# Optimization experiments

Hardware: AMD Instinct MI355X
Metric: run time of the kernel (lower is better)

The kernel has to match this reference:

```python
import jax, jax.numpy as jnp
import numpy as np

L, B, D = 512, 4, 1024          # seq(atoms), batch, embed dim
H, DH = 16, 64                  # heads, head dim
FF = 4096                       # ffn hidden
HP = 32                         # encoder_pair_embed_dim
K = 256                         # pbc-expanded atoms


def _ln(x, g, b):
    m = x.mean(-1, keepdims=True)
    v = x.var(-1, keepdims=True)
    return (x - m) / jnp.sqrt(v + 1e-5) * g + b


def _rope(x, pos):
    # x: [S,B,H,DH], pos: [B,S]
    inv_freq = 1.0 / (10000.0 ** (jnp.arange(0, DH, 2, dtype=jnp.float32) / DH))
    ang = pos.astype(jnp.float32)[..., None] * inv_freq          # [B,S,DH/2]
    cos = jnp.cos(ang).transpose(1, 0, 2)[:, :, None, :]          # [S,B,1,DH/2]
    sin = jnp.sin(ang).transpose(1, 0, 2)[:, :, None, :]
    x1, x2 = jnp.split(x, 2, axis=-1)
    return jnp.concatenate([x1 * cos - x2 * sin, x1 * sin + x2 * cos], axis=-1)


def setup_inputs() -> dict:
    key = jax.random.key(0)
    ks = jax.random.split(key, 12)
    s = 0.02
    return dict(
        x=jax.random.normal(ks[0], (L, B, D), jnp.float32),
        x_pair=jax.random.normal(ks[1], (L, L + K, B, HP), jnp.float32),
        padding_mask=jnp.zeros((B, L), bool),
        expand_mask=jnp.zeros((B, K), bool),
        position_ids=jnp.tile(jnp.arange(L, dtype=jnp.int32)[None, :], (B, 1)),
        outcell_index=jax.random.randint(ks[2], (B, K), 0, L, dtype=jnp.int32),
        wq=jax.random.normal(ks[3], (D, D), jnp.float32) * s,
        wk=jax.random.normal(ks[4], (D, D), jnp.float32) * s,
        wv=jax.random.normal(ks[5], (D, D), jnp.float32) * s,
        wo=jax.random.normal(ks[6], (D, D), jnp.float32) * s,
        fc1=jax.random.normal(ks[7], (D, FF), jnp.float32) * s,
        fc2=jax.random.normal(ks[8], (FF, D), jnp.float32) * s,
        top_ln_g=jnp.ones((D,), jnp.float32), top_ln_b=jnp.zeros((D,), jnp.float32),
        mid_ln_g=jnp.ones((D,), jnp.float32), mid_ln_b=jnp.zeros((D,), jnp.float32),
        pair_ln_g=jnp.ones((D,), jnp.float32), pair_ln_b=jnp.zeros((D,), jnp.float32),
        pair_w1=jax.random.normal(ks[9], (D, 2 * HP), jnp.float32) * s,
        pair_w2=jax.random.normal(ks[10], (2 * HP, HP), jnp.float32) * s,
    )


def reference(x, x_pair, padding_mask, expand_mask, position_ids, outcell_index,
              wq, wk, wv, wo, fc1, fc2,
              top_ln_g, top_ln_b, mid_ln_g, mid_ln_b,
              pair_ln_g, pair_ln_b, pair_w1, pair_w2):
    barange = jnp.arange(B)
    # ---- self-attention block (pre-LN, RoPE, pbc-expanded keys/values) ----
    residual = x
    h = _ln(x, top_ln_g, top_ln_b)                               # [L,B,D]
    h_exp = h[outcell_index.T, barange[None, :], :]               # [K,B,D] gather along L per batch
    kv_src = jnp.concatenate([h, h_exp], axis=0)                  # [L+K,B,D]
    q = (h @ wq).reshape(L, B, H, DH)
    k = (kv_src @ wk).reshape(L + K, B, H, DH)
    v = (kv_src @ wv).reshape(L + K, B, H, DH)
    pos_exp = position_ids[barange[:, None], outcell_index]       # [B,K]
    pos_k = jnp.concatenate([position_ids, pos_exp], axis=1)      # [B,L+K]
    q = _rope(q, position_ids)
    k = _rope(k, pos_k)
    scores = jnp.einsum('lbhd,kbhd->bhlk', q, k) / np.sqrt(DH)    # [B,H,L,L+K]
    kp_mask = jnp.concatenate([padding_mask, expand_mask], axis=1)  # [B,L+K]
    scores = jnp.where(kp_mask[:, None, None, :], -1e9, scores)
    attn = jax.nn.softmax(scores, axis=-1)
    o = jnp.einsum('bhlk,kbhd->lbhd', attn, v).reshape(L, B, D) @ wo
    x = residual + o
    # ---- FFN block ----
    residual = x
    h = _ln(x, mid_ln_g, mid_ln_b)
    x = residual + jax.nn.gelu(h @ fc1, approximate=False) @ fc2
    # ---- pair outer product ----
    x_p_i = jax.nn.silu(_ln(x, pair_ln_g, pair_ln_b) @ pair_w1) @ pair_w2   # [L,B,HP]
    expand_x_p_i = x_p_i[outcell_index.T, barange[None, :], :]              # [K,B,HP]
    x_p_j = jnp.concatenate([x_p_i, expand_x_p_i], axis=0)                  # [L+K,B,HP]
    x_pair = x_pair + jnp.einsum('lbh,kbh->lkbh', x_p_i, x_p_j)             # [L,L+K,B,HP]
    return x, x_pair
```

## Files before the change

### kernel.cpp

```cpp
#include <hip/hip_runtime.h>
#include <math.h>


typedef __bf16 bf16x8 __attribute__((ext_vector_type(8)));
typedef float f32x4 __attribute__((ext_vector_type(4)));

__device__ __forceinline__ unsigned short f2bf(float f) {
  unsigned u = __float_as_uint(f);
  u = (u + 0x7fffu + ((u >> 16) & 1u)) >> 16;
  return (unsigned short)u;
}
__device__ __forceinline__ float bf2f(unsigned short s) {
  return __uint_as_float(((unsigned)s) << 16);
}

__device__ __forceinline__ void gload_lds16(const void* g, void* l) {
  __builtin_amdgcn_global_load_lds(
      (__attribute__((address_space(1))) void*)g,
      (__attribute__((address_space(3))) void*)l, 16, 0, 0);
}

__global__ __launch_bounds__(256) void transpose_all(
    const float* __restrict__ wq, const float* __restrict__ wk, const float* __restrict__ wv,
    const float* __restrict__ wo, const float* __restrict__ fc1, const float* __restrict__ fc2,
    unsigned short* __restrict__ qkvT, unsigned short* __restrict__ woT,
    unsigned short* __restrict__ fc1T, unsigned short* __restrict__ fc2T) {
  int id = blockIdx.x;
  const float* W; unsigned short* WT; int Kd, Nd, n0, k0;
  if (id < 3072) {
    int which = id >> 10, lid = id & 1023;
    W = which == 0 ? wq : (which == 1 ? wk : wv);
    WT = qkvT + (long)which * 1024 * 1024;
    Kd = 1024; Nd = 1024; n0 = (lid & 31) * 32; k0 = (lid >> 5) * 32;
  } else if (id < 4096) {
    int lid = id - 3072;
    W = wo; WT = woT; Kd = 1024; Nd = 1024;
    n0 = (lid & 31) * 32; k0 = (lid >> 5) * 32;
  } else if (id < 8192) {
    int lid = id - 4096;
    W = fc1; WT = fc1T; Kd = 1024; Nd = 4096;
    n0 = (lid & 127) * 32; k0 = (lid >> 7) * 32;
  } else {
    int lid = id - 8192;
    W = fc2; WT = fc2T; Kd = 4096; Nd = 1024;
    n0 = (lid & 31) * 32; k0 = (lid >> 5) * 32;
  }
  __shared__ float tile[32][33];
  const int tx = threadIdx.x, ty = threadIdx.y;
#pragma unroll
  for (int i = 0; i < 32; i += 8)
    tile[ty + i][tx] = W[(long)(k0 + ty + i) * Nd + n0 + tx];
  __syncthreads();
#pragma unroll
  for (int i = 0; i < 32; i += 8)
    WT[(long)(n0 + ty + i) * Kd + k0 + tx] = f2bf(tile[tx][ty + i]);
}

__global__ __launch_bounds__(256) void ln_bf16(
    const float* __restrict__ X, unsigned short* __restrict__ Y,
    const float* __restrict__ g, const float* __restrict__ bb) {
  const int row = blockIdx.x, t = threadIdx.x;
  const float* xr = X + (long)row * 1024;
  float v[4]; float s = 0.f, ss = 0.f;
#pragma unroll
  for (int i = 0; i < 4; i++) { v[i] = xr[t + 256 * i]; s += v[i]; ss += v[i] * v[i]; }
#pragma unroll
  for (int o = 32; o > 0; o >>= 1) { s += __shfl_down(s, o); ss += __shfl_down(ss, o); }
  __shared__ float red[8];
  const int wave = t >> 6, lane = t & 63;
  if (lane == 0) { red[wave] = s; red[4 + wave] = ss; }
  __syncthreads();
  s = red[0] + red[1] + red[2] + red[3];
  ss = red[4] + red[5] + red[6] + red[7];
  const float mean = s * (1.f / 1024.f);
  const float rstd = rsqrtf(ss * (1.f / 1024.f) - mean * mean + 1e-5f);
#pragma unroll
  for (int i = 0; i < 4; i++) {
    const int c = t + 256 * i;
    Y[(long)row * 1024 + c] = f2bf((v[i] - mean) * rstd * g[c] + bb[c]);
  }
}

__global__ __launch_bounds__(256) void red_ln(
    const float* __restrict__ p0, const float* __restrict__ p1,
    const float* __restrict__ R, float* __restrict__ Xout,
    const float* __restrict__ g, const float* __restrict__ bb,
    unsigned short* __restrict__ Y) {
  const int row = blockIdx.x, t = threadIdx.x;
  const long base = (long)row * 1024;
  float v[4]; float s = 0.f, ss = 0.f;
#pragma unroll
  for (int i = 0; i < 4; i++) {
    const int c = t + 256 * i;
    float val = p0[base + c] + p1[base + c] + R[base + c];
    Xout[base + c] = val;
    v[i] = val; s += val; ss += val * val;
  }
#pragma unroll
  for (int o = 32; o > 0; o >>= 1) { s += __shfl_down(s, o); ss += __shfl_down(ss, o); }
  __shared__ float red[8];
  const int wave = t >> 6, lane = t & 63;
  if (lane == 0) { red[wave] = s; red[4 + wave] = ss; }
  __syncthreads();
  s = red[0] + red[1] + red[2] + red[3];
  ss = red[4] + red[5] + red[6] + red[7];
  const float mean = s * (1.f / 1024.f);
  const float rstd = rsqrtf(ss * (1.f / 1024.f) - mean * mean + 1e-5f);
#pragma unroll
  for (int i = 0; i < 4; i++) {
    const int c = t + 256 * i;
    Y[base + c] = f2bf((v[i] - mean) * rstd * g[c] + bb[c]);
  }
}

__global__ __launch_bounds__(256) void gather_kv(unsigned short* kv, const int* __restrict__ oc) {
  int idx = blockIdx.x * 256 + threadIdx.x;
  int col4 = idx & 255;
  int r = idx >> 8;
  int j = r >> 2, b = r & 3;
  int src = oc[b * 256 + j] * 4 + b;
  ((ushort4*)kv)[((512 + j) * 4 + b) * 256 + col4] = ((const ushort4*)kv)[src * 256 + col4];
}

template <int EPI>
__global__ __launch_bounds__(256) void gemm_nt(
    const unsigned short* __restrict__ A, const unsigned short* __restrict__ BT,
    void* __restrict__ Cout, const float* __restrict__ R, int M, int N, int Kd) {
  __shared__ __align__(16) unsigned short As[128 * 32];
  __shared__ __align__(16) unsigned short Bs[128 * 32];
  const int t = threadIdx.x;
  const int wave = t >> 6, lane = t & 63;
  const int m0 = blockIdx.y * 128, n0 = blockIdx.x * 128;
  const int wr = wave >> 1, wc = wave & 1;
  const int lr = lane & 15, lg = lane >> 4;

  f32x4 acc[4][4] = {};

  const int srow = 32 * wave + (lane >> 2);
  const int schunk = (lane & 3) * 8;
  const unsigned short* Ag = A + (long)(m0 + srow) * Kd + schunk;
  const unsigned short* Bg = BT + (long)(n0 + srow) * Kd + schunk;
  unsigned short* AsW = &As[(32 * wave) * 32];
  unsigned short* BsW = &Bs[(32 * wave) * 32];

  for (int k0 = 0; k0 < Kd; k0 += 32) {
    __syncthreads();
    gload_lds16(Ag + k0, AsW);
    gload_lds16(Ag + k0 + 16 * (long)Kd, AsW + 16 * 32);
    gload_lds16(Bg + k0, BsW);
    gload_lds16(Bg + k0 + 16 * (long)Kd, BsW + 16 * 32);
    asm volatile("s_waitcnt vmcnt(0)" ::: "memory");
    __syncthreads();

    bf16x8 af[4], bfr[4];
#pragma unroll
    for (int mf = 0; mf < 4; mf++)
      af[mf] = *(const bf16x8*)&As[(64 * wr + 16 * mf + lr) * 32 + lg * 8];
#pragma unroll
    for (int nf = 0; nf < 4; nf++)
      bfr[nf] = *(const bf16x8*)&Bs[(64 * wc + 16 * nf + lr) * 32 + lg * 8];
#pragma unroll
    for (int mf = 0; mf < 4; mf++)
#pragma unroll
      for (int nf = 0; nf < 4; nf++)
        acc[mf][nf] = __builtin_amdgcn_mfma_f32_16x16x32_bf16(af[mf], bfr[nf], acc[mf][nf], 0, 0, 0);
  }

#pragma unroll
  for (int mf = 0; mf < 4; mf++)
#pragma unroll
    for (int nf = 0; nf < 4; nf++)
#pragma unroll
      for (int r = 0; r < 4; r++) {
        const int row = m0 + 64 * wr + 16 * mf + 4 * lg + r;
        const int col = n0 + 64 * wc + 16 * nf + lr;
        const long off = (long)row * N + col;
        float v = acc[mf][nf][r];
        if constexpr (EPI == 1) {
          ((float*)Cout)[off] = v + R[off];
        } else if constexpr (EPI == 2) {
          float gl = 0.5f * v * (1.0f + erff(v * 0.70710678118654752f));
          ((unsigned short*)Cout)[off] = f2bf(gl);
        } else if constexpr (EPI == 3) {
          ((unsigned short*)Cout)[off] = f2bf(v);
        } else {
          ((float*)Cout)[off] = v;
        }
      }
}

__global__ __launch_bounds__(256) void gemm_nt_splitk(
    const unsigned short* __restrict__ A, const unsigned short* __restrict__ BT,
    float* __restrict__ Cp, int M, int N, int Kd) {
  const int kh = Kd >> 1;
  const long kbase = (long)blockIdx.z * kh;
  const unsigned short* A2 = A + kbase;
  const unsigned short* B2 = BT + kbase;
  float* Cz = Cp + (long)blockIdx.z * M * N;

  __shared__ __align__(16) unsigned short As[128 * 32];
  __shared__ __align__(16) unsigned short Bs[128 * 32];
  const int t = threadIdx.x;
  const int wave = t >> 6, lane = t & 63;
  const int m0 = blockIdx.y * 128, n0 = blockIdx.x * 128;
  const int wr = wave >> 1, wc = wave & 1;
  const int lr = lane & 15, lg = lane >> 4;

  f32x4 acc[4][4] = {};

  const int srow = 32 * wave + (lane >> 2);
  const int schunk = (lane & 3) * 8;
  const unsigned short* Ag = A2 + (long)(m0 + srow) * Kd + schunk;
  const unsigned short* Bg = B2 + (long)(n0 + srow) * Kd + schunk;
  unsigned short* AsW = &As[(32 * wave) * 32];
  unsigned short* BsW = &Bs[(32 * wave) * 32];

  for (int k0 = 0; k0 < kh; k0 += 32) {
    __syncthreads();
    gload_lds16(Ag + k0, AsW);
    gload_lds16(Ag + k0 + 16 * (long)Kd, AsW + 16 * 32);
    gload_lds16(Bg + k0, BsW);
    gload_lds16(Bg + k0 + 16 * (long)Kd, BsW + 16 * 32);
    asm volatile("s_waitcnt vmcnt(0)" ::: "memory");
    __syncthreads();

    bf16x8 af[4], bfr[4];
#pragma unroll
    for (int mf = 0; mf < 4; mf++)
      af[mf] = *(const bf16x8*)&As[(64 * wr + 16 * mf + lr) * 32 + lg * 8];
#pragma unroll
    for (int nf = 0; nf < 4; nf++)
      bfr[nf] = *(const bf16x8*)&Bs[(64 * wc + 16 * nf + lr) * 32 + lg * 8];
#pragma unroll
    for (int mf = 0; mf < 4; mf++)
#pragma unroll
      for (int nf = 0; nf < 4; nf++)
        acc[mf][nf] = __builtin_amdgcn_mfma_f32_16x16x32_bf16(af[mf], bfr[nf], acc[mf][nf], 0, 0, 0);
  }

#pragma unroll
  for (int mf = 0; mf < 4; mf++)
#pragma unroll
    for (int nf = 0; nf < 4; nf++)
#pragma unroll
      for (int r = 0; r < 4; r++) {
        const int row = m0 + 64 * wr + 16 * mf + 4 * lg + r;
        const int col = n0 + 64 * wc + 16 * nf + lr;
        Cz[(long)row * N + col] = acc[mf][nf][r];
      }
}

__global__ __launch_bounds__(256) void rope_split2(
    const unsigned short* __restrict__ QKV, const int* __restrict__ pos_ids,
    const int* __restrict__ oc,
    unsigned short* __restrict__ qb, unsigned short* __restrict__ kbh) {
  int idx = blockIdx.x * 256 + threadIdx.x;
  bool isq = idx < 1048576;
  int rp = isq ? idx : idx - 1048576;
  int p = rp & 511;
  int row = rp >> 9;
  int hh = p >> 5, dp = p & 31;
  int s = row >> 2, b = row & 3;
  int pos = isq ? pos_ids[b * 512 + s]
                : ((s < 512) ? pos_ids[b * 512 + s]
                             : pos_ids[b * 512 + oc[b * 256 + s - 512]]);
  const unsigned short* src = QKV + (long)row * 3072 + (isq ? 0 : 1024) + hh * 64 + dp;
  float x1 = bf2f(src[0]), x2 = bf2f(src[32]);
  float invf = exp2f((float)dp * -0.41524101186091903f);
  float ang = (float)pos * invf;
  float sn = sinf(ang), cs = cosf(ang);
  float o1 = x1 * cs - x2 * sn, o2 = x1 * sn + x2 * cs;
  if (isq) {
    unsigned short* dst = qb + ((long)(b * 16 + hh) * 512 + s) * 64 + dp;
    dst[0] = f2bf(o1 * 0.125f); dst[32] = f2bf(o2 * 0.125f);
  } else {
    unsigned short* dst = kbh + ((long)(b * 16 + hh) * 768 + s) * 64 + dp;
    dst[0] = f2bf(o1); dst[32] = f2bf(o2);
  }
}

__global__ __launch_bounds__(256) void v_transpose(
    const unsigned short* __restrict__ QKV, unsigned short* __restrict__ vth) {
  const int kt = blockIdx.x, bh = blockIdx.y;
  const int b = bh >> 4, h = bh & 15;
  __shared__ unsigned short tile[64][72];
  const int t = threadIdx.x;
  const int key = t >> 2, c = t & 3;
  const unsigned short* src = QKV + ((long)(kt * 64 + key) * 4 + b) * 3072 + 2048 + h * 64 + c * 16;
#pragma unroll
  for (int j = 0; j < 16; j++) tile[c * 16 + j][key] = src[j];
  __syncthreads();
  const int d = t >> 2;
  unsigned short* dst = vth + ((long)bh * 64 + d) * 768 + kt * 64 + c * 16;
  *(uint4*)dst = *(const uint4*)&tile[d][c * 16];
  *(uint4*)(dst + 8) = *(const uint4*)&tile[d][c * 16 + 8];
}

__global__ __launch_bounds__(512) void att_mfma(
    const unsigned short* __restrict__ qb, const unsigned short* __restrict__ kbh,
    const unsigned short* __restrict__ vth,
    const unsigned char* __restrict__ pad_mask, const unsigned char* __restrict__ exp_mask,
    unsigned short* __restrict__ o_bf) {
  const int bh = blockIdx.y, b = bh >> 4, h = bh & 15;
  const int q0 = blockIdx.x * 128;
  const int t = threadIdx.x, wave = t >> 6, lane = t & 63;
  const int lr = lane & 15, lg = lane >> 4;

  __shared__ __align__(16) unsigned short Ks[64][72];
  __shared__ __align__(16) unsigned short Vs[64][72];
  __shared__ __align__(16) unsigned short Ps[8][16][72];
  __shared__ float maskAdd[768];

  for (int i = t; i < 768; i += 512)
    maskAdd[i] = ((i < 512) ? pad_mask[b * 512 + i] : exp_mask[b * 256 + i - 512]) ? -1e9f : 0.f;

  const unsigned short* qrow = qb + ((long)bh * 512 + q0 + wave * 16 + lr) * 64;
  const bf16x8 aq0 = *(const bf16x8*)(qrow + lg * 8);
  const bf16x8 aq1 = *(const bf16x8*)(qrow + 32 + lg * 8);

  float m_run[4] = {-1e30f, -1e30f, -1e30f, -1e30f};
  float l_run[4] = {0.f, 0.f, 0.f, 0.f};
  f32x4 Oacc[4] = {};

  const int srow = t >> 3, sc = (t & 7) * 8;
  for (int kt = 0; kt < 12; ++kt) {
    __syncthreads();
    *(uint4*)&Ks[srow][sc] =
        *(const uint4*)(kbh + ((long)bh * 768 + kt * 64 + srow) * 64 + sc);
    *(uint4*)&Vs[srow][sc] =
        *(const uint4*)(vth + ((long)bh * 64 + srow) * 768 + kt * 64 + sc);
    __syncthreads();

    float sv[4][4];
#pragma unroll
    for (int nf = 0; nf < 4; nf++) {
      f32x4 z = {};
      bf16x8 b0 = *(const bf16x8*)&Ks[nf * 16 + lr][lg * 8];
      bf16x8 b1 = *(const bf16x8*)&Ks[nf * 16 + lr][32 + lg * 8];
      z = __builtin_amdgcn_mfma_f32_16x16x32_bf16(aq0, b0, z, 0, 0, 0);
      z = __builtin_amdgcn_mfma_f32_16x16x32_bf16(aq1, b1, z, 0, 0, 0);
      float ma = maskAdd[kt * 64 + nf * 16 + lr];
#pragma unroll
      for (int r = 0; r < 4; r++) sv[nf][r] = z[r] + ma;
    }
    float mnew[4], scale[4], rs[4];
#pragma unroll
    for (int r = 0; r < 4; r++) {
      float tm = fmaxf(fmaxf(sv[0][r], sv[1][r]), fmaxf(sv[2][r], sv[3][r]));
      tm = fmaxf(tm, __shfl_xor(tm, 1));
      tm = fmaxf(tm, __shfl_xor(tm, 2));
      tm = fmaxf(tm, __shfl_xor(tm, 4));
      tm = fmaxf(tm, __shfl_xor(tm, 8));
      mnew[r] = fmaxf(m_run[r], tm);
      scale[r] = __expf(m_run[r] - mnew[r]);
      m_run[r] = mnew[r];
      rs[r] = 0.f;
    }
#pragma unroll
    for (int nf = 0; nf < 4; nf++)
#pragma unroll
      for (int r = 0; r < 4; r++) {
        float p = __expf(sv[nf][r] - mnew[r]);
        rs[r] += p;
        Ps[wave][lg * 4 + r][nf * 16 + lr] = f2bf(p);
      }
#pragma unroll
    for (int r = 0; r < 4; r++) {
      float x = rs[r];
      x += __shfl_xor(x, 1); x += __shfl_xor(x, 2);
      x += __shfl_xor(x, 4); x += __shfl_xor(x, 8);
      l_run[r] = l_run[r] * scale[r] + x;
#pragma unroll
      for (int nf = 0; nf < 4; nf++) Oacc[nf][r] *= scale[r];
    }
    bf16x8 ap0 = *(const bf16x8*)&Ps[wave][lr][lg * 8];
    bf16x8 ap1 = *(const bf16x8*)&Ps[wave][lr][32 + lg * 8];
#pragma unroll
    for (int nf = 0; nf < 4; nf++) {
      bf16x8 b0 = *(const bf16x8*)&Vs[nf * 16 + lr][lg * 8];
      bf16x8 b1 = *(const bf16x8*)&Vs[nf * 16 + lr][32 + lg * 8];
      Oacc[nf] = __builtin_amdgcn_mfma_f32_16x16x32_bf16(ap0, b0, Oacc[nf], 0, 0, 0);
      Oacc[nf] = __builtin_amdgcn_mfma_f32_16x16x32_bf16(ap1, b1, Oacc[nf], 0, 0, 0);
    }
  }

#pragma unroll
  for (int r = 0; r < 4; r++) {
    float inv = 1.0f / l_run[r];
    int l = q0 + wave * 16 + lg * 4 + r;
#pragma unroll
    for (int nf = 0; nf < 4; nf++)
      o_bf[(((long)l * 4 + b) * 16 + h) * 64 + nf * 16 + lr] = f2bf(Oacc[nf][r] * inv);
  }
}

__global__ __launch_bounds__(256) void pair_head(
    const unsigned short* __restrict__ pln, const float* __restrict__ w1,
    const float* __restrict__ w2, float* __restrict__ xpi) {
  const int row = blockIdx.x, t = threadIdx.x;
  __shared__ float red[64][4];
  __shared__ float s1[64];
  const int c = t & 63, qt = t >> 6;
  const unsigned short* xr = pln + (long)row * 1024;
  float acc = 0.f;
  for (int k = qt * 256; k < qt * 256 + 256; k++)
    acc += bf2f(xr[k]) * w1[k * 64 + c];
  red[c][qt] = acc;
  __syncthreads();
  if (t < 64) {
    float v = red[t][0] + red[t][1] + red[t][2] + red[t][3];
    s1[t] = v / (1.f + __expf(-v));
  }
  __syncthreads();
  if (t < 32) {
    float o = 0.f;
    for (int k = 0; k < 64; k++) o += s1[k] * w2[k * 32 + t];
    xpi[(long)row * 32 + t] = o;
  }
}

__global__ __launch_bounds__(256) void pair_update(
    const float* __restrict__ x_pair, const float* __restrict__ xpi,
    const int* __restrict__ oc, float* __restrict__ out) {
  int idx4 = blockIdx.x * 256 + threadIdx.x;
  int h4 = idx4 & 7;
  int lkb = idx4 >> 3;
  int b = lkb & 3;
  int lk = lkb >> 2;
  int kk = lk % 768;
  int l = lk / 768;
  int src = (kk < 512) ? kk : oc[b * 256 + kk - 512];
  float4 pv = ((const float4*)x_pair)[idx4];
  float4 a = ((const float4*)xpi)[(l * 4 + b) * 8 + h4];
  float4 bb = ((const float4*)xpi)[(src * 4 + b) * 8 + h4];
  float4 o;
  o.x = pv.x + a.x * bb.x; o.y = pv.y + a.y * bb.y;
  o.z = pv.z + a.z * bb.z; o.w = pv.w + a.w * bb.w;
  ((float4*)out)[idx4] = o;
}

extern "C" void kernel_launch(void* const* d_in, const int* in_sizes, int n_in,
                              void* d_out, int out_size, void* d_ws, size_t ws_size,
                              hipStream_t stream) {
  const float* x        = (const float*)d_in[0];
  const float* x_pair   = (const float*)d_in[1];
  const unsigned char* pad_mask = (const unsigned char*)d_in[2];
  const unsigned char* exp_mask = (const unsigned char*)d_in[3];
  const int* pos_ids    = (const int*)d_in[4];
  const int* oc         = (const int*)d_in[5];
  const float* wq  = (const float*)d_in[6];
  const float* wk  = (const float*)d_in[7];
  const float* wv  = (const float*)d_in[8];
  const float* wo  = (const float*)d_in[9];
  const float* fc1 = (const float*)d_in[10];
  const float* fc2 = (const float*)d_in[11];
  const float* tln_g = (const float*)d_in[12];
  const float* tln_b = (const float*)d_in[13];
  const float* mln_g = (const float*)d_in[14];
  const float* mln_b = (const float*)d_in[15];
  const float* pln_g = (const float*)d_in[16];
  const float* pln_b = (const float*)d_in[17];
  const float* w1 = (const float*)d_in[18];
  const float* w2 = (const float*)d_in[19];

  char* wsp = (char*)d_ws;
  size_t off = 0;
  auto alloc = [&](size_t bytes) -> void* {
    void* p = wsp + off;
    off = (off + bytes + 255) & ~(size_t)255;
    return p;
  };
  unsigned short* qkvT = (unsigned short*)alloc(3072LL * 1024 * 2);
  unsigned short* woT  = (unsigned short*)alloc(1024LL * 1024 * 2);
  unsigned short* fc1T = (unsigned short*)alloc(4096LL * 1024 * 2);
  unsigned short* fc2T = (unsigned short*)alloc(1024LL * 4096 * 2);
  unsigned short* kvb  = (unsigned short*)alloc(3072LL * 1024 * 2);
  unsigned short* QKVb = (unsigned short*)alloc(3072LL * 3072 * 2);
  unsigned short* qb   = (unsigned short*)alloc(64LL * 512 * 64 * 2);
  unsigned short* kbh  = (unsigned short*)alloc(64LL * 768 * 64 * 2);
  unsigned short* vth  = (unsigned short*)alloc(64LL * 64 * 768 * 2);
  unsigned short* obf  = (unsigned short*)alloc(2048LL * 1024 * 2);
  float* x1            = (float*)alloc(2048LL * 1024 * 4);
  unsigned short* h2   = (unsigned short*)alloc(2048LL * 1024 * 2);
  unsigned short* gbf  = (unsigned short*)alloc(2048LL * 4096 * 2);
  unsigned short* plnb = (unsigned short*)alloc(2048LL * 1024 * 2);
  float* xpi           = (float*)alloc(2048LL * 32 * 4);
  float* pp            = (float*)alloc(2LL * 2048 * 1024 * 4);
  (void)ws_size; (void)in_sizes; (void)n_in; (void)out_size;

  dim3 tb(32, 8);
  transpose_all<<<12288, tb, 0, stream>>>(wq, wk, wv, wo, fc1, fc2,
                                          qkvT, woT, fc1T, fc2T);

  ln_bf16<<<2048, 256, 0, stream>>>(x, kvb, tln_g, tln_b);
  gather_kv<<<1024, 256, 0, stream>>>(kvb, oc);

  gemm_nt<3><<<dim3(24, 24), 256, 0, stream>>>(kvb, qkvT, QKVb, nullptr, 3072, 3072, 1024);

  rope_split2<<<10240, 256, 0, stream>>>(QKVb, pos_ids, oc, qb, kbh);
  v_transpose<<<dim3(12, 64), 256, 0, stream>>>(QKVb, vth);

  att_mfma<<<dim3(4, 64), 512, 0, stream>>>(qb, kbh, vth, pad_mask, exp_mask, obf);

  gemm_nt_splitk<<<dim3(8, 16, 2), 256, 0, stream>>>(obf, woT, pp, 2048, 1024, 1024);
  red_ln<<<2048, 256, 0, stream>>>(pp, pp + 2097152, x, x1, mln_g, mln_b, h2);

  gemm_nt<2><<<dim3(32, 16), 256, 0, stream>>>(h2, fc1T, gbf, nullptr, 2048, 4096, 1024);

  gemm_nt_splitk<<<dim3(8, 16, 2), 256, 0, stream>>>(gbf, fc2T, pp, 2048, 1024, 4096);
  red_ln<<<2048, 256, 0, stream>>>(pp, pp + 2097152, x1, (float*)d_out, pln_g, pln_b, plnb);

  pair_head<<<2048, 256, 0, stream>>>(plnb, w1, w2, xpi);
  pair_update<<<49152, 256, 0, stream>>>(x_pair, xpi, oc, (float*)d_out + 2097152);
}
```

Baseline: 324.9 us.

## Skip unused QKV tiles, fuse pair head into LN, widen transpose, drop attention LDS staging

Adds a dedicated QKV GEMM that launches only the tiles actually consumed: full 3072 columns for the first 2048 rows, and only the K/V columns for the expanded-atom rows, so no Q projection is computed for those rows. Fuses the pair-head MLP into the residual+LayerNorm kernel, removing the bf16 LN output buffer and one launch. The weight-transpose kernel now handles 64x32 tiles with paired bf16 stores, halving the block count. The attention kernel reads K and V fragments directly from global memory instead of staging them through shared memory, trading two barriers per key tile for uncached, less coalesced global loads.

```diff
diff --git a/kernel.cpp b/kernel.cpp
--- a/kernel.cpp
+++ b/kernel.cpp
@@ -27,33 +27,34 @@
     unsigned short* __restrict__ fc1T, unsigned short* __restrict__ fc2T) {
   int id = blockIdx.x;
   const float* W; unsigned short* WT; int Kd, Nd, n0, k0;
-  if (id < 3072) {
-    int which = id >> 10, lid = id & 1023;
-    W = which == 0 ? wq : (which == 1 ? wk : wv);
-    WT = qkvT + (long)which * 1024 * 1024;
-    Kd = 1024; Nd = 1024; n0 = (lid & 31) * 32; k0 = (lid >> 5) * 32;
+  if (id < 2048) {
+    int which = id >> 9, lid = id & 511;
+    W = which == 0 ? wq : (which == 1 ? wk : (which == 2 ? wv : wo));
+    WT = which < 3 ? qkvT + (long)which * 1024 * 1024 : woT;
+    Kd = 1024; Nd = 1024;
+    k0 = (lid >> 5) * 64; n0 = (lid & 31) * 32;
   } else if (id < 4096) {
-    int lid = id - 3072;
-    W = wo; WT = woT; Kd = 1024; Nd = 1024;
-    n0 = (lid & 31) * 32; k0 = (lid >> 5) * 32;
-  } else if (id < 8192) {
+    int lid = id - 2048;
+    W = fc1; WT = fc1T; Kd = 1024; Nd = 4096;
+    k0 = (lid >> 7) * 64; n0 = (lid & 127) * 32;
+  } else {
     int lid = id - 4096;
-    W = fc1; WT = fc1T; Kd = 1024; Nd = 4096;
-    n0 = (lid & 127) * 32; k0 = (lid >> 7) * 32;
-  } else {
-    int lid = id - 8192;
     W = fc2; WT = fc2T; Kd = 4096; Nd = 1024;
-    n0 = (lid & 31) * 32; k0 = (lid >> 5) * 32;
-  }
-  __shared__ float tile[32][33];
+    k0 = (lid >> 5) * 64; n0 = (lid & 31) * 32;
+  }
+  __shared__ float tile[64][33];
   const int tx = threadIdx.x, ty = threadIdx.y;
 #pragma unroll
-  for (int i = 0; i < 32; i += 8)
-    tile[ty + i][tx] = W[(long)(k0 + ty + i) * Nd + n0 + tx];
-  __syncthreads();
-#pragma unroll
-  for (int i = 0; i < 32; i += 8)
-    WT[(long)(n0 + ty + i) * Kd + k0 + tx] = f2bf(tile[tx][ty + i]);
+  for (int j = 0; j < 64; j += 8)
+    tile[ty + j][tx] = W[(long)(k0 + ty + j) * Nd + n0 + tx];
+  __syncthreads();
+#pragma unroll
+  for (int i = 0; i < 32; i += 8) {
+    ushort2 o;
+    o.x = f2bf(tile[2 * tx][ty + i]);
+    o.y = f2bf(tile[2 * tx + 1][ty + i]);
+    *(ushort2*)&WT[(long)(n0 + ty + i) * Kd + k0 + 2 * tx] = o;
+  }
 }
 
 __global__ __launch_bounds__(256) void ln_bf16(
@@ -110,6 +111,59 @@
   for (int i = 0; i < 4; i++) {
     const int c = t + 256 * i;
     Y[base + c] = f2bf((v[i] - mean) * rstd * g[c] + bb[c]);
+  }
+}
+
+__global__ __launch_bounds__(256) void red_ln_pair(
+    const float* __restrict__ p0, const float* __restrict__ p1,
+    const float* __restrict__ R, float* __restrict__ Xout,
+    const float* __restrict__ g, const float* __restrict__ bb,
+    const float* __restrict__ w1, const float* __restrict__ w2,
+    float* __restrict__ xpi) {
+  const int row = blockIdx.x, t = threadIdx.x;
+  const long base = (long)row * 1024;
+  __shared__ float lnrow[1024];
+  __shared__ float red[8];
+  __shared__ float red2[64][4];
+  __shared__ float s1[64];
+  float v[4]; float s = 0.f, ss = 0.f;
+#pragma unroll
+  for (int i = 0; i < 4; i++) {
+    const int c = t + 256 * i;
+    float val = p0[base + c] + p1[base + c] + R[base + c];
+    Xout[base + c] = val;
+    v[i] = val; s += val; ss += val * val;
+  }
+#pragma unroll
+  for (int o = 32; o > 0; o >>= 1) { s += __shfl_down(s, o); ss += __shfl_down(ss, o); }
+  const int wave = t >> 6, lane = t & 63;
+  if (lane == 0) { red[wave] = s; red[4 + wave] = ss; }
+  __syncthreads();
+  s = red[0] + red[1] + red[2] + red[3];
+  ss = red[4] + red[5] + red[6] + red[7];
+  const float mean = s * (1.f / 1024.f);
+  const float rstd = rsqrtf(ss * (1.f / 1024.f) - mean * mean + 1e-5f);
+#pragma unroll
+  for (int i = 0; i < 4; i++) {
+    const int c = t + 256 * i;
+    lnrow[c] = (v[i] - mean) * rstd * g[c] + bb[c];
+  }
+  __syncthreads();
+  const int c = t & 63, qt = t >> 6;
+  float acc = 0.f;
+  for (int k = qt * 256; k < qt * 256 + 256; k++)
+    acc += lnrow[k] * w1[k * 64 + c];
+  red2[c][qt] = acc;
+  __syncthreads();
+  if (t < 64) {
+    float vv = red2[t][0] + red2[t][1] + red2[t][2] + red2[t][3];
+    s1[t] = vv / (1.f + __expf(-vv));
+  }
+  __syncthreads();
+  if (t < 32) {
+    float o = 0.f;
+    for (int k = 0; k < 64; k++) o += s1[k] * w2[k * 32 + t];
+    xpi[(long)row * 32 + t] = o;
   }
 }
 
@@ -186,6 +240,67 @@
         } else {
           ((float*)Cout)[off] = v;
         }
+      }
+}
+
+__global__ __launch_bounds__(256) void gemm_qkv(
+    const unsigned short* __restrict__ A, const unsigned short* __restrict__ BT,
+    unsigned short* __restrict__ Cout) {
+  constexpr int N = 3072, Kd = 1024;
+  int bid = blockIdx.x;
+  int mt, nt;
+  if (bid < 384) { mt = bid / 24; nt = bid % 24; }
+  else { int rem = bid - 384; mt = 16 + (rem >> 4); nt = 8 + (rem & 15); }
+  const int m0 = mt * 128, n0 = nt * 128;
+
+  __shared__ __align__(16) unsigned short As[128 * 32];
+  __shared__ __align__(16) unsigned short Bs[128 * 32];
+  const int t = threadIdx.x;
+  const int wave = t >> 6, lane = t & 63;
+  const int wr = wave >> 1, wc = wave & 1;
+  const int lr = lane & 15, lg = lane >> 4;
+
+  f32x4 acc[4][4] = {};
+
+  const int srow = 32 * wave + (lane >> 2);
+  const int schunk = (lane & 3) * 8;
+  const unsigned short* Ag = A + (long)(m0 + srow) * Kd + schunk;
+  const unsigned short* Bg = BT + (long)(n0 + srow) * Kd + schunk;
+  unsigned short* AsW = &As[(32 * wave) * 32];
+  unsigned short* BsW = &Bs[(32 * wave) * 32];
+
+  for (int k0 = 0; k0 < Kd; k0 += 32) {
+    __syncthreads();
+    gload_lds16(Ag + k0, AsW);
+    gload_lds16(Ag + k0 + 16 * (long)Kd, AsW + 16 * 32);
+    gload_lds16(Bg + k0, BsW);
+    gload_lds16(Bg + k0 + 16 * (long)Kd, BsW + 16 * 32);
+    asm volatile("s_waitcnt vmcnt(0)" ::: "memory");
+    __syncthreads();
+
+    bf16x8 af[4], bfr[4];
+#pragma unroll
+    for (int mf = 0; mf < 4; mf++)
+      af[mf] = *(const bf16x8*)&As[(64 * wr + 16 * mf + lr) * 32 + lg * 8];
+#pragma unroll
+    for (int nf = 0; nf < 4; nf++)
+      bfr[nf] = *(const bf16x8*)&Bs[(64 * wc + 16 * nf + lr) * 32 + lg * 8];
+#pragma unroll
+    for (int mf = 0; mf < 4; mf++)
+#pragma unroll
+      for (int nf = 0; nf < 4; nf++)
+        acc[mf][nf] = __builtin_amdgcn_mfma_f32_16x16x32_bf16(af[mf], bfr[nf], acc[mf][nf], 0, 0, 0);
+  }
+
+#pragma unroll
+  for (int mf = 0; mf < 4; mf++)
+#pragma unroll
+    for (int nf = 0; nf < 4; nf++)
+#pragma unroll
+      for (int r = 0; r < 4; r++) {
+        const int row = m0 + 64 * wr + 16 * mf + 4 * lg + r;
+        const int col = n0 + 64 * wc + 16 * nf + lr;
+        Cout[(long)row * N + col] = f2bf(acc[mf][nf][r]);
       }
 }
 
@@ -306,8 +421,6 @@
   const int t = threadIdx.x, wave = t >> 6, lane = t & 63;
   const int lr = lane & 15, lg = lane >> 4;
 
-  __shared__ __align__(16) unsigned short Ks[64][72];
-  __shared__ __align__(16) unsigned short Vs[64][72];
   __shared__ __align__(16) unsigned short Ps[8][16][72];
   __shared__ float maskAdd[768];
 
@@ -317,26 +430,23 @@
   const unsigned short* qrow = qb + ((long)bh * 512 + q0 + wave * 16 + lr) * 64;
   const bf16x8 aq0 = *(const bf16x8*)(qrow + lg * 8);
   const bf16x8 aq1 = *(const bf16x8*)(qrow + 32 + lg * 8);
+  __syncthreads();
 
   float m_run[4] = {-1e30f, -1e30f, -1e30f, -1e30f};
   float l_run[4] = {0.f, 0.f, 0.f, 0.f};
   f32x4 Oacc[4] = {};
 
-  const int srow = t >> 3, sc = (t & 7) * 8;
+  const unsigned short* kb0 = kbh + (long)bh * 768 * 64;
+  const unsigned short* vb0 = vth + (long)bh * 64 * 768;
+
   for (int kt = 0; kt < 12; ++kt) {
-    __syncthreads();
-    *(uint4*)&Ks[srow][sc] =
-        *(const uint4*)(kbh + ((long)bh * 768 + kt * 64 + srow) * 64 + sc);
-    *(uint4*)&Vs[srow][sc] =
-        *(const uint4*)(vth + ((long)bh * 64 + srow) * 768 + kt * 64 + sc);
-    __syncthreads();
-
     float sv[4][4];
 #pragma unroll
     for (int nf = 0; nf < 4; nf++) {
+      const unsigned short* kr = kb0 + (long)(kt * 64 + nf * 16 + lr) * 64;
       f32x4 z = {};
-      bf16x8 b0 = *(const bf16x8*)&Ks[nf * 16 + lr][lg * 8];
-      bf16x8 b1 = *(const bf16x8*)&Ks[nf * 16 + lr][32 + lg * 8];
+      bf16x8 b0 = *(const bf16x8*)(kr + lg * 8);
+      bf16x8 b1 = *(const bf16x8*)(kr + 32 + lg * 8);
       z = __builtin_amdgcn_mfma_f32_16x16x32_bf16(aq0, b0, z, 0, 0, 0);
       z = __builtin_amdgcn_mfma_f32_16x16x32_bf16(aq1, b1, z, 0, 0, 0);
       float ma = maskAdd[kt * 64 + nf * 16 + lr];
@@ -377,8 +487,9 @@
     bf16x8 ap1 = *(const bf16x8*)&Ps[wave][lr][32 + lg * 8];
 #pragma unroll
     for (int nf = 0; nf < 4; nf++) {
-      bf16x8 b0 = *(const bf16x8*)&Vs[nf * 16 + lr][lg * 8];
-      bf16x8 b1 = *(const bf16x8*)&Vs[nf * 16 + lr][32 + lg * 8];
+      const unsigned short* vr = vb0 + (long)(nf * 16 + lr) * 768 + kt * 64;
+      bf16x8 b0 = *(const bf16x8*)(vr + lg * 8);
+      bf16x8 b1 = *(const bf16x8*)(vr + 32 + lg * 8);
       Oacc[nf] = __builtin_amdgcn_mfma_f32_16x16x32_bf16(ap0, b0, Oacc[nf], 0, 0, 0);
       Oacc[nf] = __builtin_amdgcn_mfma_f32_16x16x32_bf16(ap1, b1, Oacc[nf], 0, 0, 0);
     }
@@ -391,31 +502,6 @@
 #pragma unroll
     for (int nf = 0; nf < 4; nf++)
       o_bf[(((long)l * 4 + b) * 16 + h) * 64 + nf * 16 + lr] = f2bf(Oacc[nf][r] * inv);
-  }
-}
-
-__global__ __launch_bounds__(256) void pair_head(
-    const unsigned short* __restrict__ pln, const float* __restrict__ w1,
-    const float* __restrict__ w2, float* __restrict__ xpi) {
-  const int row = blockIdx.x, t = threadIdx.x;
-  __shared__ float red[64][4];
-  __shared__ float s1[64];
-  const int c = t & 63, qt = t >> 6;
-  const unsigned short* xr = pln + (long)row * 1024;
-  float acc = 0.f;
-  for (int k = qt * 256; k < qt * 256 + 256; k++)
-    acc += bf2f(xr[k]) * w1[k * 64 + c];
-  red[c][qt] = acc;
-  __syncthreads();
-  if (t < 64) {
-    float v = red[t][0] + red[t][1] + red[t][2] + red[t][3];
-    s1[t] = v / (1.f + __expf(-v));
-  }
-  __syncthreads();
-  if (t < 32) {
-    float o = 0.f;
-    for (int k = 0; k < 64; k++) o += s1[k] * w2[k * 32 + t];
-    xpi[(long)row * 32 + t] = o;
   }
 }
 
@@ -483,19 +569,18 @@
   float* x1            = (float*)alloc(2048LL * 1024 * 4);
   unsigned short* h2   = (unsigned short*)alloc(2048LL * 1024 * 2);
   unsigned short* gbf  = (unsigned short*)alloc(2048LL * 4096 * 2);
-  unsigned short* plnb = (unsigned short*)alloc(2048LL * 1024 * 2);
   float* xpi           = (float*)alloc(2048LL * 32 * 4);
   float* pp            = (float*)alloc(2LL * 2048 * 1024 * 4);
   (void)ws_size; (void)in_sizes; (void)n_in; (void)out_size;
 
   dim3 tb(32, 8);
-  transpose_all<<<12288, tb, 0, stream>>>(wq, wk, wv, wo, fc1, fc2,
-                                          qkvT, woT, fc1T, fc2T);
+  transpose_all<<<6144, tb, 0, stream>>>(wq, wk, wv, wo, fc1, fc2,
+                                         qkvT, woT, fc1T, fc2T);
 
   ln_bf16<<<2048, 256, 0, stream>>>(x, kvb, tln_g, tln_b);
   gather_kv<<<1024, 256, 0, stream>>>(kvb, oc);
 
-  gemm_nt<3><<<dim3(24, 24), 256, 0, stream>>>(kvb, qkvT, QKVb, nullptr, 3072, 3072, 1024);
+  gemm_qkv<<<512, 256, 0, stream>>>(kvb, qkvT, QKVb);
 
   rope_split2<<<10240, 256, 0, stream>>>(QKVb, pos_ids, oc, qb, kbh);
   v_transpose<<<dim3(12, 64), 256, 0, stream>>>(QKVb, vth);
@@ -508,8 +593,8 @@
   gemm_nt<2><<<dim3(32, 16), 256, 0, stream>>>(h2, fc1T, gbf, nullptr, 2048, 4096, 1024);
 
   gemm_nt_splitk<<<dim3(8, 16, 2), 256, 0, stream>>>(gbf, fc2T, pp, 2048, 1024, 4096);
-  red_ln<<<2048, 256, 0, stream>>>(pp, pp + 2097152, x1, (float*)d_out, pln_g, pln_b, plnb);
-
-  pair_head<<<2048, 256, 0, stream>>>(plnb, w1, w2, xpi);
+  red_ln_pair<<<2048, 256, 0, stream>>>(pp, pp + 2097152, x1, (float*)d_out,
+                                        pln_g, pln_b, w1, w2, xpi);
+
   pair_update<<<49152, 256, 0, stream>>>(x_pair, xpi, oc, (float*)d_out + 2097152);
 }
```

Measured after the change: 318.2 us. 2.1% less time.
